# Performance work log

Hardware: AMD Instinct MI355X
Metric: run time of the kernel (lower is better)

Reference implementation:

```python
import jax, jax.numpy as jnp
import numpy as np

C = 1.0
TAU = 1.0
LE = 1.0
LH = 1.0
LN_EPS = 1e-5

def _safe_norm(x, keepdims=False):
    return jnp.clip(jnp.sqrt(jnp.sum(x * x, axis=-1, keepdims=keepdims)), 1e-15)

def _project_to_ball(x, c, eps=1e-5):
    sqrt_c = c ** 0.5
    norm = _safe_norm(x, keepdims=True)
    max_norm = (1.0 - eps) / sqrt_c
    scale = jnp.where(norm > max_norm, max_norm / norm, 1.0)
    return x * scale

def _lambda_x(x, c):
    x = _project_to_ball(x, c)
    x2 = jnp.sum(x * x, axis=-1, keepdims=True)
    return 2.0 / jnp.clip(1.0 - c * x2, 1e-15)

def _mobius_add(x, y, c):
    x = _project_to_ball(x, c)
    y = _project_to_ball(y, c)
    x2 = jnp.sum(x * x, axis=-1, keepdims=True)
    y2 = jnp.sum(y * y, axis=-1, keepdims=True)
    xy = jnp.sum(x * y, axis=-1, keepdims=True)
    num = (1 + 2 * c * xy + c * y2) * x + (1 - c * x2) * y
    den = 1 + 2 * c * xy + c ** 2 * x2 * y2
    return num / jnp.clip(den, 1e-15)

def _exp_map_x(x, v, c):
    sqrt_c = c ** 0.5
    lam = _lambda_x(x, c)
    vnorm = _safe_norm(v, keepdims=True)
    v_dir = v / vnorm
    factor = jnp.tanh(lam * sqrt_c * vnorm / 2.0) / sqrt_c
    out = _mobius_add(x, v_dir * factor, c)
    return _project_to_ball(out, c)

def _log_map_x(x, y, c):
    sqrt_c = c ** 0.5
    lam = _lambda_x(x, c)
    u = _mobius_add(-x, y, c)
    unorm = _safe_norm(u, keepdims=True)
    u_dir = u / unorm
    arg = jnp.minimum(sqrt_c * unorm, 1 - 1e-7)
    scale = 2.0 / (lam * sqrt_c) * jnp.arctanh(arg)
    return scale * u_dir

def _poincare_distance_sq(x, y, c):
    sqrt_c = c ** 0.5
    x = _project_to_ball(x, c)
    y = _project_to_ball(y, c)
    diff = _mobius_add(-x, y, c)
    norm = _safe_norm(diff, keepdims=False)
    arg = jnp.minimum(sqrt_c * norm, 1 - 1e-7)
    dist = 2.0 / sqrt_c * jnp.arctanh(arg)
    return dist * dist

def setup_inputs() -> dict:
    key = jax.random.key(0)
    ks = jax.random.split(key, 6)
    B, N, L, A, de, dh, z_dim = 8, 8, 64, 64, 128, 64, 128
    z_e, z_h = z_dim // 2 + z_dim % 2, z_dim // 2
    return {
        "curr_rho_batch": jax.random.normal(ks[0], (B, A, de), jnp.float32),
        "curr_hyp_emb": 0.1 * jax.random.normal(ks[1], (B, dh), jnp.float32),
        "demo_rho_batch": jax.random.normal(ks[2], (B, N, L, A, de), jnp.float32),
        "demo_hyp_emb": 0.1 * jax.random.normal(ks[3], (B, N, L, dh), jnp.float32),
        "We": 0.02 * jax.random.normal(ks[4], (z_e, de), jnp.float32),
        "Wh": 0.02 * jax.random.normal(ks[5], (z_h, dh), jnp.float32),
        "ln_gamma": jnp.ones((z_dim,), jnp.float32),
        "ln_beta": jnp.zeros((z_dim,), jnp.float32),
    }

def reference(curr_rho_batch, curr_hyp_emb, demo_rho_batch, demo_hyp_emb, We, Wh, ln_gamma, ln_beta):
    B, A, de = curr_rho_batch.shape
    _, N, L, _, _ = demo_rho_batch.shape
    M = N * L
    dh = curr_hyp_emb.shape[-1]
    demo_rho_flat = demo_rho_batch.reshape(B, M, A, de)   # [B,M,A,de]
    demo_hyp_flat = demo_hyp_emb.reshape(B, M, dh)        # [B,M,dh]
    # Euclidean squared distances: [B,M,A] -> [B,A,M]
    e_diff_sq = jnp.sum((curr_rho_batch[:, None, :, :] - demo_rho_flat) ** 2, axis=-1)
    e_diff_sq = jnp.transpose(e_diff_sq, (0, 2, 1))
    # Hyperbolic squared distances: [B,M]
    dH2 = _poincare_distance_sq(curr_hyp_emb[:, None, :], demo_hyp_flat, C)
    scores = -(LH * dH2[:, None, :] + LE * e_diff_sq) / max(TAU, 1e-8)  # [B,A,M]
    alpha = jax.nn.softmax(scores, axis=-1)
    # Euclidean aggregation
    e_out = jnp.einsum('bam,bmad->bad', alpha, demo_rho_flat)  # [B,A,de]
    # Hyperbolic Karcher-mean step
    log_vecs = _log_map_x(curr_hyp_emb[:, None, :], demo_hyp_flat, C)  # [B,M,dh]
    v = jnp.einsum('bam,bmd->bad', alpha, log_vecs)  # [B,A,dh]
    x_ba = jnp.broadcast_to(curr_hyp_emb[:, None, :], (B, A, dh))
    h_out = _exp_map_x(x_ba, v, C)  # [B,A,dh]
    z = jnp.concatenate([e_out @ We.T, h_out @ Wh.T], axis=-1)  # [B,A,z_dim]
    mean = jnp.mean(z, axis=-1, keepdims=True)
    var = jnp.var(z, axis=-1, keepdims=True)
    z = (z - mean) / jnp.sqrt(var + LN_EPS) * ln_gamma + ln_beta
    return z
```

## Files before the change

### kernel.cpp

```cpp
#include <hip/hip_runtime.h>

#define DEV __device__ __forceinline__

constexpr int A_ = 64, DE = 128, M_ = 512, DH = 64;

DEV float wred_sum64(float v) {
#pragma unroll
    for (int o = 1; o < 64; o <<= 1) v += __shfl_xor(v, o, 64);
    return v;
}

__global__ __launch_bounds__(256) void k_hyp(const float* __restrict__ curr_hyp,
                                             const float* __restrict__ demo_hyp,
                                             float* __restrict__ dH2,
                                             float* __restrict__ logv) {
    const int lane = threadIdx.x & 63;
    const int r    = (blockIdx.x << 2) + (threadIdx.x >> 6);
    const int b    = r >> 9;

    float x = curr_hyp[(b << 6) + lane];
    float y = demo_hyp[((size_t)r << 6) + lane];
    const float mx = 1.0f - 1e-5f;

    float x2r = wred_sum64(x * x);
    float xn  = fmaxf(sqrtf(x2r), 1e-15f);
    float sx  = xn > mx ? mx / xn : 1.0f;
    x *= sx;
    float x2 = x2r * sx * sx;
    float y2r = wred_sum64(y * y);
    float yn  = fmaxf(sqrtf(y2r), 1e-15f);
    float sy  = yn > mx ? mx / yn : 1.0f;
    y *= sy;
    float y2 = y2r * sy * sy;

    float xy = wred_sum64(x * y);
    float num = (1.f - 2.f * xy + y2) * (-x) + (1.f - x2) * y;
    float den = fmaxf(1.f - 2.f * xy + x2 * y2, 1e-15f);
    float u   = num / den;

    float u2  = wred_sum64(u * u);
    float un  = fmaxf(sqrtf(u2), 1e-15f);
    float arg = fminf(un, 1.f - 1e-7f);
    float at  = 0.5f * __logf((1.f + arg) / (1.f - arg));

    if (lane == 0) dH2[r] = 4.f * at * at;

    float lamden = fmaxf(1.f - x2, 1e-15f);
    float ls     = lamden * at / un;
    logv[((size_t)r << 6) + lane] = ls * u;
}

__global__ __launch_bounds__(512, 4) void k_main(const float* __restrict__ curr_rho,
                                                 const float* __restrict__ demo_rho,
                                                 const float* __restrict__ curr_hyp,
                                                 const float* __restrict__ dH2,
                                                 const float* __restrict__ logv,
                                                 const float* __restrict__ We,
                                                 const float* __restrict__ Wh,
                                                 const float* __restrict__ gamma,
                                                 const float* __restrict__ beta,
                                                 float* __restrict__ out) {
    __shared__ __align__(16) float buf[2][32 * 132];
    __shared__ float lds_sc[512];
    __shared__ float lds_dh[512];
    __shared__ float redmax[8];
    __shared__ float redsum[8];
    __shared__ float vpart[8][64];
    __shared__ float eh[192];

    const int t    = threadIdx.x;
    const int lane = t & 63;
    const int wv   = t >> 6;
    const int dp   = t & 15;
    const int mi   = t >> 4;
    const int blk  = blockIdx.x;
    const int b    = blk >> 6, a = blk & 63;

    lds_dh[t] = dH2[(b << 9) + t];

    float qf[8];
    {
        float4 q0 = *(const float4*)(curr_rho + (size_t)blk * DE + dp * 8);
        float4 q1 = *(const float4*)(curr_rho + (size_t)blk * DE + dp * 8 + 4);
        qf[0] = q0.x; qf[1] = q0.y; qf[2] = q0.z; qf[3] = q0.w;
        qf[4] = q1.x; qf[5] = q1.y; qf[6] = q1.z; qf[7] = q1.w;
    }

    const size_t rowStride = (size_t)A_ * DE;
    const float* base_ba = demo_rho + ((size_t)b * M_ * A_ + a) * DE;
    const int r0 = t >> 5, part = t & 31;

    {
        float4 s0 = *(const float4*)(base_ba + (size_t)r0 * rowStride + part * 4);
        float4 s1 = *(const float4*)(base_ba + (size_t)(r0 + 16) * rowStride + part * 4);
        *(float4*)&buf[0][r0 * 132 + part * 4]        = s0;
        *(float4*)&buf[0][(r0 + 16) * 132 + part * 4] = s1;
    }

    float e_acc[8];
#pragma unroll
    for (int j = 0; j < 8; j++) e_acc[j] = 0.f;
    float gmax = -1e30f, gsum = 0.f;

    for (int c = 0; c < 16; ++c) {
        const int cur = c & 1;
        float4 n0, n1;
        if (c < 15) {
            const float* dbase = base_ba + (size_t)(c + 1) * 32 * rowStride;
            n0 = *(const float4*)(dbase + (size_t)r0 * rowStride + part * 4);
            n1 = *(const float4*)(dbase + (size_t)(r0 + 16) * rowStride + part * 4);
        }
        __syncthreads();

        float kf[8];
        {
            float4 k0 = *(const float4*)&buf[cur][mi * 132 + dp * 8];
            float4 k1 = *(const float4*)&buf[cur][mi * 132 + dp * 8 + 4];
            kf[0] = k0.x; kf[1] = k0.y; kf[2] = k0.z; kf[3] = k0.w;
            kf[4] = k1.x; kf[5] = k1.y; kf[6] = k1.z; kf[7] = k1.w;
        }
        float ps = 0.f;
#pragma unroll
        for (int j = 0; j < 8; j++) { float d = qf[j] - kf[j]; ps += d * d; }
        ps += __shfl_xor(ps, 1, 64);
        ps += __shfl_xor(ps, 2, 64);
        ps += __shfl_xor(ps, 4, 64);
        ps += __shfl_xor(ps, 8, 64);
        float sc = -(lds_dh[c * 32 + mi] + ps);
        if (dp == 0) lds_sc[c * 32 + mi] = sc;

        float lm = fmaxf(sc, __shfl_xor(sc, 16, 64));
        lm = fmaxf(lm, __shfl_xor(lm, 32, 64));
        float wexp = __expf(sc - lm);
        float wsum = wexp + __shfl_xor(wexp, 16, 64);
        wsum += __shfl_xor(wsum, 32, 64);
        if (lane == 0) { redmax[wv] = lm; redsum[wv] = wsum; }
        __syncthreads();

        float cmax = redmax[0];
#pragma unroll
        for (int w = 1; w < 8; w++) cmax = fmaxf(cmax, redmax[w]);
        float csum = 0.f;
#pragma unroll
        for (int w = 0; w < 8; w++) csum += redsum[w] * __expf(redmax[w] - cmax);
        float gnew = fmaxf(gmax, cmax);
        float r1 = __expf(gmax - gnew);
        float r2 = __expf(cmax - gnew);
        gsum = gsum * r1 + csum * r2;
        float w = __expf(sc - gnew);
#pragma unroll
        for (int j = 0; j < 8; j++) e_acc[j] = fmaf(w, kf[j], e_acc[j] * r1);
        gmax = gnew;

        if (c < 15) {
            *(float4*)&buf[cur ^ 1][r0 * 132 + part * 4]        = n0;
            *(float4*)&buf[cur ^ 1][(r0 + 16) * 132 + part * 4] = n1;
        }
    }

    const float inv = 1.f / gsum;
    float al = __expf(lds_sc[t] - gmax) * inv;
    lds_sc[t] = al;

    float* rede = buf[0];
    *(float4*)&rede[mi * 132 + dp * 8]     = make_float4(e_acc[0], e_acc[1], e_acc[2], e_acc[3]);
    *(float4*)&rede[mi * 132 + dp * 8 + 4] = make_float4(e_acc[4], e_acc[5], e_acc[6], e_acc[7]);
    __syncthreads();
    if (t < 128) {
        float s = 0.f;
#pragma unroll
        for (int g = 0; g < 32; g++) s += rede[g * 132 + t];
        eh[t] = s * inv;
    }

    {
        const float* lvb = logv + ((size_t)(b * M_) + wv * 64) * DH;
        float acc = 0.f;
#pragma unroll 8
        for (int i = 0; i < 64; ++i)
            acc = fmaf(lds_sc[wv * 64 + i], lvb[(size_t)i * DH + lane], acc);
        vpart[wv][lane] = acc;
    }
    __syncthreads();

    if (wv == 0) {
        float v = 0.f;
#pragma unroll
        for (int w = 0; w < 8; w++) v += vpart[w][lane];

        const float mx = 1.0f - 1e-5f;
        float x = curr_hyp[(b << 6) + lane];
        float x2r = wred_sum64(x * x);
        float xn  = fmaxf(sqrtf(x2r), 1e-15f);
        float sx  = xn > mx ? mx / xn : 1.f;
        x *= sx;
        float x2 = x2r * sx * sx;
        float lamden = fmaxf(1.f - x2, 1e-15f);

        float v2 = wred_sum64(v * v);
        float vn = fmaxf(sqrtf(v2), 1e-15f);
        float targ   = vn / lamden;
        float e2     = __expf(2.f * targ);
        float factor = 1.f - 2.f / (e2 + 1.f);
        float wvv    = v * (factor / vn);

        float w2 = wred_sum64(wvv * wvv);
        float xw = wred_sum64(x * wvv);
        float num = (1.f + 2.f * xw + w2) * x + (1.f - x2) * wvv;
        float den = fmaxf(1.f + 2.f * xw + x2 * w2, 1e-15f);
        float h   = num / den;
        float h2  = wred_sum64(h * h);
        float hn  = fmaxf(sqrtf(h2), 1e-15f);
        float shh = hn > mx ? mx / hn : 1.f;
        h *= shh;
        eh[128 + lane] = h;

        float ze = 0.f;
        const float* werow = We + lane * 128;
#pragma unroll
        for (int d0 = 0; d0 < 128; d0 += 4) {
            float4 wv4 = *(const float4*)(werow + d0);
            ze = fmaf(eh[d0 + 0], wv4.x, ze);
            ze = fmaf(eh[d0 + 1], wv4.y, ze);
            ze = fmaf(eh[d0 + 2], wv4.z, ze);
            ze = fmaf(eh[d0 + 3], wv4.w, ze);
        }
        float zh = 0.f;
        const float* whrow = Wh + lane * 64;
#pragma unroll
        for (int d0 = 0; d0 < 64; d0 += 4) {
            float4 wv4 = *(const float4*)(whrow + d0);
            zh = fmaf(eh[128 + d0 + 0], wv4.x, zh);
            zh = fmaf(eh[128 + d0 + 1], wv4.y, zh);
            zh = fmaf(eh[128 + d0 + 2], wv4.z, zh);
            zh = fmaf(eh[128 + d0 + 3], wv4.w, zh);
        }
        float ssum = wred_sum64(ze + zh);
        float mean = ssum * (1.f / 128.f);
        float sq   = wred_sum64(ze * ze + zh * zh);
        float var  = sq * (1.f / 128.f) - mean * mean;
        float rinv = rsqrtf(var + 1e-5f);
        float oe = (ze - mean) * rinv * gamma[lane] + beta[lane];
        float oh = (zh - mean) * rinv * gamma[64 + lane] + beta[64 + lane];
        out[(size_t)blk * 128 + lane]      = oe;
        out[(size_t)blk * 128 + 64 + lane] = oh;
    }
}

extern "C" void kernel_launch(void* const* d_in, const int* in_sizes, int n_in,
                              void* d_out, int out_size, void* d_ws, size_t ws_size,
                              hipStream_t stream) {
    const float* curr_rho = (const float*)d_in[0];
    const float* curr_hyp = (const float*)d_in[1];
    const float* demo_rho = (const float*)d_in[2];
    const float* demo_hyp = (const float*)d_in[3];
    const float* We       = (const float*)d_in[4];
    const float* Wh       = (const float*)d_in[5];
    const float* gamma    = (const float*)d_in[6];
    const float* beta     = (const float*)d_in[7];
    float* out = (float*)d_out;

    float* ws   = (float*)d_ws;
    float* dH2  = ws;
    float* logv = ws + 4096;

    k_hyp<<<1024, 256, 0, stream>>>(curr_hyp, demo_hyp, dH2, logv);
    k_main<<<512, 512, 0, stream>>>(curr_rho, demo_rho, curr_hyp, dH2, logv,
                                    We, Wh, gamma, beta, out);
}
```

Measured before the change: 211.7 us.

## Stream demo rows directly to registers with per-lane online softmax, drop LDS staging

Replaces the shared-memory double-buffered chunk loop, which needed two block-wide barriers per chunk, with each wave streaming its own 64 demo rows straight from global memory into registers. Each lane keeps its own online-softmax state, and the states are merged by a shuffle reduction and then a single cross-wave reduction. The alpha computation is folded into the log-vector accumulation, and the large LDS buffer is removed, which lowers shared-memory use. The cost is more exp calls per lane and shuffle traffic for merging the accumulators.

```diff
diff --git a/kernel.cpp b/kernel.cpp
--- a/kernel.cpp
+++ b/kernel.cpp
@@ -60,19 +60,19 @@
                                                  const float* __restrict__ gamma,
                                                  const float* __restrict__ beta,
                                                  float* __restrict__ out) {
-    __shared__ __align__(16) float buf[2][32 * 132];
     __shared__ float lds_sc[512];
     __shared__ float lds_dh[512];
     __shared__ float redmax[8];
     __shared__ float redsum[8];
+    __shared__ __align__(16) float accbuf[8 * 132];
     __shared__ float vpart[8][64];
     __shared__ float eh[192];
 
     const int t    = threadIdx.x;
     const int lane = t & 63;
     const int wv   = t >> 6;
-    const int dp   = t & 15;
-    const int mi   = t >> 4;
+    const int dp   = lane & 15;
+    const int mq   = lane >> 4;
     const int blk  = blockIdx.x;
     const int b    = blk >> 6, a = blk & 63;
 
@@ -87,99 +87,97 @@
     }
 
     const size_t rowStride = (size_t)A_ * DE;
-    const float* base_ba = demo_rho + ((size_t)b * M_ * A_ + a) * DE;
-    const int r0 = t >> 5, part = t & 31;
-
-    {
-        float4 s0 = *(const float4*)(base_ba + (size_t)r0 * rowStride + part * 4);
-        float4 s1 = *(const float4*)(base_ba + (size_t)(r0 + 16) * rowStride + part * 4);
-        *(float4*)&buf[0][r0 * 132 + part * 4]        = s0;
-        *(float4*)&buf[0][(r0 + 16) * 132 + part * 4] = s1;
-    }
-
-    float e_acc[8];
-#pragma unroll
-    for (int j = 0; j < 8; j++) e_acc[j] = 0.f;
-    float gmax = -1e30f, gsum = 0.f;
-
-    for (int c = 0; c < 16; ++c) {
-        const int cur = c & 1;
+    const float* p = demo_rho + (((size_t)b * M_ + wv * 64 + mq) * A_ + a) * DE + dp * 8;
+
+    float mx = -1e30f, sm = 0.f, ac[8];
+#pragma unroll
+    for (int j = 0; j < 8; j++) ac[j] = 0.f;
+
+    float4 c0 = *(const float4*)p;
+    float4 c1 = *(const float4*)(p + 4);
+
+    for (int i = 0; i < 16; ++i) {
+        const float* pn = p + 4 * rowStride;
         float4 n0, n1;
-        if (c < 15) {
-            const float* dbase = base_ba + (size_t)(c + 1) * 32 * rowStride;
-            n0 = *(const float4*)(dbase + (size_t)r0 * rowStride + part * 4);
-            n1 = *(const float4*)(dbase + (size_t)(r0 + 16) * rowStride + part * 4);
-        }
-        __syncthreads();
+        if (i < 15) { n0 = *(const float4*)pn; n1 = *(const float4*)(pn + 4); }
 
         float kf[8];
-        {
-            float4 k0 = *(const float4*)&buf[cur][mi * 132 + dp * 8];
-            float4 k1 = *(const float4*)&buf[cur][mi * 132 + dp * 8 + 4];
-            kf[0] = k0.x; kf[1] = k0.y; kf[2] = k0.z; kf[3] = k0.w;
-            kf[4] = k1.x; kf[5] = k1.y; kf[6] = k1.z; kf[7] = k1.w;
-        }
+        kf[0] = c0.x; kf[1] = c0.y; kf[2] = c0.z; kf[3] = c0.w;
+        kf[4] = c1.x; kf[5] = c1.y; kf[6] = c1.z; kf[7] = c1.w;
+
         float ps = 0.f;
 #pragma unroll
-        for (int j = 0; j < 8; j++) { float d = qf[j] - kf[j]; ps += d * d; }
+        for (int j = 0; j < 8; j++) { float d = qf[j] - kf[j]; ps = fmaf(d, d, ps); }
         ps += __shfl_xor(ps, 1, 64);
         ps += __shfl_xor(ps, 2, 64);
         ps += __shfl_xor(ps, 4, 64);
         ps += __shfl_xor(ps, 8, 64);
-        float sc = -(lds_dh[c * 32 + mi] + ps);
-        if (dp == 0) lds_sc[c * 32 + mi] = sc;
-
-        float lm = fmaxf(sc, __shfl_xor(sc, 16, 64));
-        lm = fmaxf(lm, __shfl_xor(lm, 32, 64));
-        float wexp = __expf(sc - lm);
-        float wsum = wexp + __shfl_xor(wexp, 16, 64);
-        wsum += __shfl_xor(wsum, 32, 64);
-        if (lane == 0) { redmax[wv] = lm; redsum[wv] = wsum; }
-        __syncthreads();
-
-        float cmax = redmax[0];
-#pragma unroll
-        for (int w = 1; w < 8; w++) cmax = fmaxf(cmax, redmax[w]);
-        float csum = 0.f;
-#pragma unroll
-        for (int w = 0; w < 8; w++) csum += redsum[w] * __expf(redmax[w] - cmax);
-        float gnew = fmaxf(gmax, cmax);
-        float r1 = __expf(gmax - gnew);
-        float r2 = __expf(cmax - gnew);
-        gsum = gsum * r1 + csum * r2;
-        float w = __expf(sc - gnew);
-#pragma unroll
-        for (int j = 0; j < 8; j++) e_acc[j] = fmaf(w, kf[j], e_acc[j] * r1);
-        gmax = gnew;
-
-        if (c < 15) {
-            *(float4*)&buf[cur ^ 1][r0 * 132 + part * 4]        = n0;
-            *(float4*)&buf[cur ^ 1][(r0 + 16) * 132 + part * 4] = n1;
+
+        const int ml = wv * 64 + mq + 4 * i;
+        float sc = -(lds_dh[ml] + ps);
+        if (dp == 0) lds_sc[ml] = sc;
+
+        float nm = fmaxf(mx, sc);
+        float r  = __expf(mx - nm);
+        float w  = __expf(sc - nm);
+        sm = sm * r + w;
+#pragma unroll
+        for (int j = 0; j < 8; j++) ac[j] = fmaf(ac[j], r, w * kf[j]);
+        mx = nm;
+
+        p = pn; c0 = n0; c1 = n1;
+    }
+
+#pragma unroll
+    for (int off = 16; off < 64; off <<= 1) {
+        float mxo = __shfl_xor(mx, off, 64);
+        float smo = __shfl_xor(sm, off, 64);
+        float aco[8];
+#pragma unroll
+        for (int j = 0; j < 8; j++) aco[j] = __shfl_xor(ac[j], off, 64);
+        float nm = fmaxf(mx, mxo);
+        float r1 = __expf(mx - nm), r2 = __expf(mxo - nm);
+        sm = sm * r1 + smo * r2;
+#pragma unroll
+        for (int j = 0; j < 8; j++) ac[j] = ac[j] * r1 + aco[j] * r2;
+        mx = nm;
+    }
+    if (lane == 0) { redmax[wv] = mx; redsum[wv] = sm; }
+    __syncthreads();
+
+    float gmax = redmax[0];
+#pragma unroll
+    for (int w = 1; w < 8; w++) gmax = fmaxf(gmax, redmax[w]);
+    float gsum = 0.f;
+#pragma unroll
+    for (int w = 0; w < 8; w++) gsum += redsum[w] * __expf(redmax[w] - gmax);
+    const float inv = 1.f / gsum;
+
+    float resc = __expf(mx - gmax);
+    if (lane < 16) {
+        *(float4*)&accbuf[wv * 132 + dp * 8] =
+            make_float4(ac[0] * resc, ac[1] * resc, ac[2] * resc, ac[3] * resc);
+        *(float4*)&accbuf[wv * 132 + dp * 8 + 4] =
+            make_float4(ac[4] * resc, ac[5] * resc, ac[6] * resc, ac[7] * resc);
+    }
+
+    {
+        const float* lvb = logv + ((size_t)(b * M_) + wv * 64) * DH;
+        float vacc = 0.f;
+#pragma unroll 8
+        for (int i = 0; i < 64; ++i) {
+            float al = __expf(lds_sc[wv * 64 + i] - gmax);
+            vacc = fmaf(al, lvb[(size_t)i * DH + lane], vacc);
         }
-    }
-
-    const float inv = 1.f / gsum;
-    float al = __expf(lds_sc[t] - gmax) * inv;
-    lds_sc[t] = al;
-
-    float* rede = buf[0];
-    *(float4*)&rede[mi * 132 + dp * 8]     = make_float4(e_acc[0], e_acc[1], e_acc[2], e_acc[3]);
-    *(float4*)&rede[mi * 132 + dp * 8 + 4] = make_float4(e_acc[4], e_acc[5], e_acc[6], e_acc[7]);
+        vpart[wv][lane] = vacc * inv;
+    }
     __syncthreads();
+
     if (t < 128) {
         float s = 0.f;
 #pragma unroll
-        for (int g = 0; g < 32; g++) s += rede[g * 132 + t];
+        for (int g = 0; g < 8; g++) s += accbuf[g * 132 + t];
         eh[t] = s * inv;
-    }
-
-    {
-        const float* lvb = logv + ((size_t)(b * M_) + wv * 64) * DH;
-        float acc = 0.f;
-#pragma unroll 8
-        for (int i = 0; i < 64; ++i)
-            acc = fmaf(lds_sc[wv * 64 + i], lvb[(size_t)i * DH + lane], acc);
-        vpart[wv][lane] = acc;
     }
     __syncthreads();
 
@@ -188,11 +186,11 @@
 #pragma unroll
         for (int w = 0; w < 8; w++) v += vpart[w][lane];
 
-        const float mx = 1.0f - 1e-5f;
+        const float mxb = 1.0f - 1e-5f;
         float x = curr_hyp[(b << 6) + lane];
         float x2r = wred_sum64(x * x);
         float xn  = fmaxf(sqrtf(x2r), 1e-15f);
-        float sx  = xn > mx ? mx / xn : 1.f;
+        float sx  = xn > mxb ? mxb / xn : 1.f;
         x *= sx;
         float x2 = x2r * sx * sx;
         float lamden = fmaxf(1.f - x2, 1e-15f);
@@ -211,7 +209,7 @@
         float h   = num / den;
         float h2  = wred_sum64(h * h);
         float hn  = fmaxf(sqrtf(h2), 1e-15f);
-        float shh = hn > mx ? mx / hn : 1.f;
+        float shh = hn > mxb ? mxb / hn : 1.f;
         h *= shh;
         eh[128 + lane] = h;
 
```

New measurement: 230.9 us. 1.09x slower.
